# Optimization experiments

Measured on AMD Instinct MI355X. Metric: run time of the kernel, lower is better.

## Reference

```python
import jax, jax.numpy as jnp
import numpy as np

NUM_HEADS = 32
HEAD_DIM = 128
NUM_KV_HEADS = 8
SCALE = 1.0 / np.sqrt(HEAD_DIM)
BATCH = 8
SEQ = 1024
TOTAL = BATCH * SEQ


def setup_inputs() -> dict:
    key = jax.random.key(0)
    kq, kk, kv = jax.random.split(key, 3)
    q = jax.random.normal(kq, (TOTAL, NUM_HEADS * HEAD_DIM), dtype=jnp.float32)
    k = jax.random.normal(kk, (TOTAL, NUM_KV_HEADS * HEAD_DIM), dtype=jnp.float32)
    v = jax.random.normal(kv, (TOTAL, NUM_KV_HEADS * HEAD_DIM), dtype=jnp.float32)
    cu = (jnp.arange(BATCH + 1, dtype=jnp.int32) * SEQ)
    return {"q": q, "k": k, "v": v, "cu_seqlens_q": cu, "cu_seqlens_k": cu}


def reference(q, k, v, cu_seqlens_q, cu_seqlens_k):
    # Prefill path of Attention.forward: causal varlen GQA flash attention.
    # Equal-length sequences -> reshape flat tokens into [B, S, ...].
    B = cu_seqlens_q.shape[0] - 1          # static: number of sequences
    T = q.shape[0]
    S = T // B
    G = NUM_HEADS // NUM_KV_HEADS          # query heads per kv head
    qr = q.reshape(B, S, NUM_KV_HEADS, G, HEAD_DIM)
    kr = k.reshape(B, S, NUM_KV_HEADS, HEAD_DIM)
    vr = v.reshape(B, S, NUM_KV_HEADS, HEAD_DIM)
    # scores: [B, Hkv, G, Sq, Sk]
    scores = jnp.einsum('bqhgd,bkhd->bhgqk', qr, kr) * jnp.float32(SCALE)
    causal = jnp.tril(jnp.ones((S, S), dtype=bool))  # [Sq, Sk]
    scores = jnp.where(causal, scores, jnp.finfo(scores.dtype).min)
    probs = jax.nn.softmax(scores, axis=-1)
    o = jnp.einsum('bhgqk,bkhd->bqhgd', probs, vr)
    return o.reshape(T, NUM_HEADS * HEAD_DIM)
```

## Files before the change

kernel.cpp:

```cpp
#include <hip/hip_runtime.h>
#include <hip/hip_bf16.h>
#include <stdint.h>

typedef __bf16 bf16_t;
typedef __attribute__((ext_vector_type(8))) __bf16 bf16x8;
typedef __attribute__((ext_vector_type(4))) __bf16 bf16x4;
typedef __attribute__((ext_vector_type(4))) float f32x4;

#define NHEADS 32
#define HDIM 128
#define NKV 8
#define GQ 4
#define BATCH 8
#define SEQ 1024
#define TOTAL (BATCH * SEQ)
#define QD (NHEADS * HDIM)
#define KVD (NKV * HDIM)
#define ATT_SCALE 0.08838834764831845f
#define QSCL (0.08838834764831845f * 1.4426950408889634f)

#define QBLK 64
#define KBLK 64
#define NQT (SEQ / QBLK)

__device__ __forceinline__ void gload16(const bf16_t* g, bf16_t* l) {
    __builtin_amdgcn_global_load_lds(
        (const __attribute__((address_space(1))) void*)g,
        (__attribute__((address_space(3))) void*)l,
        16, 0, 0);
}

__device__ __forceinline__ uint32_t cvt_pk_bf16(float lo, float hi) {
    uint32_t r;
    asm("v_cvt_pk_bf16_f32 %0, %1, %2" : "=v"(r) : "v"(lo), "v"(hi));
    return r;
}

__global__ __launch_bounds__(256)
void attn_prepass_kernel(const float* __restrict__ kg, const float* __restrict__ vg,
                         bf16_t* __restrict__ kws, bf16_t* __restrict__ vtws)
{
    const int bid = blockIdx.x;
    const int tid = threadIdx.x;
    if (bid < 512) {
        __shared__ bf16_t Lt[128 * 130];
        const int b  = bid >> 6;
        const int hk = (bid >> 3) & 7;
        const int tt = bid & 7;
        const float* vp = vg + ((long)(b * SEQ + tt * 128)) * KVD + hk * HDIM;
        #pragma unroll
        for (int it = 0; it < 16; ++it) {
            int idx = it * 256 + tid;
            int t  = idx >> 5;
            int c4 = (idx & 31) * 4;
            float4 f = *(const float4*)(vp + (long)t * KVD + c4);
            Lt[(c4 + 0) * 130 + t] = (bf16_t)f.x;
            Lt[(c4 + 1) * 130 + t] = (bf16_t)f.y;
            Lt[(c4 + 2) * 130 + t] = (bf16_t)f.z;
            Lt[(c4 + 3) * 130 + t] = (bf16_t)f.w;
        }
        __syncthreads();
        bf16_t* op = vtws + ((long)((b * NKV + hk) * HDIM)) * SEQ + tt * 128;
        #pragma unroll
        for (int jt = 0; jt < 8; ++jt) {
            int jdx = jt * 256 + tid;
            int d  = jdx >> 4;
            int c8 = (jdx & 15) * 8;
            const bf16_t* lp = &Lt[d * 130 + c8];
            uint32_t u0 = *(const uint32_t*)(lp + 0);
            uint32_t u1 = *(const uint32_t*)(lp + 2);
            uint32_t u2 = *(const uint32_t*)(lp + 4);
            uint32_t u3 = *(const uint32_t*)(lp + 6);
            int kl0 = c8 & 63;
            int p0  = (kl0 & 32) | ((kl0 & 8) << 1) | ((kl0 & 16) >> 2);
            bf16_t* dst = op + (long)d * SEQ + (c8 & ~63);
            uint2 lo; lo.x = u0; lo.y = u1;
            uint2 hi; hi.x = u2; hi.y = u3;
            *(uint2*)(dst + p0)     = lo;
            *(uint2*)(dst + p0 + 8) = hi;
        }
    } else {
        const long total4 = (long)TOTAL * KVD / 4;
        const float4* k4 = (const float4*)kg;
        for (long i = (long)(bid - 512) * 256 + tid; i < total4; i += 1024L * 256) {
            float4 f = k4[i];
            bf16x4 o4;
            o4[0] = (bf16_t)f.x; o4[1] = (bf16_t)f.y;
            o4[2] = (bf16_t)f.z; o4[3] = (bf16_t)f.w;
            *(bf16x4*)(kws + i * 4) = o4;
        }
    }
}

__global__ __launch_bounds__(512, 4)
void attn_fwd_v11(const float* __restrict__ qg, const bf16_t* __restrict__ kws,
                  const bf16_t* __restrict__ vtws, float* __restrict__ og)
{
    __shared__ __align__(16) bf16_t Kl[2][KBLK * HDIM];
    __shared__ __align__(16) bf16_t Vl[2][HDIM * KBLK];

    const int tid  = threadIdx.x;
    const int w    = tid >> 6;
    const int lane = tid & 63;
    const int l16  = lane & 15;
    const int l4   = lane >> 4;

    const int bid = blockIdx.x;
    const int hg  = bid & 1;
    const int bh  = (bid >> 1) & 63;
    const int pi  = bid >> 7;
    const int b   = bh >> 3;
    const int hk  = bh & 7;
    const int g2  = w >> 2;
    const int fs  = w & 3;
    const int h   = hk * GQ + hg * 2 + g2;

    const bf16_t* kbase = kws + (long)(b * SEQ) * KVD + hk * HDIM;
    const bf16_t* vbase = vtws + (long)((b * NKV + hk) * HDIM) * SEQ;
    const int kc0 = w * 2;

    long koff[2], voff[2];
    int ldst[2];
    #pragma unroll
    for (int i = 0; i < 2; ++i) {
        int c = kc0 + i;
        int r = c * 4 + (lane >> 4);
        koff[i] = (long)r * KVD + (((lane & 15) ^ (r & 7)) * 8);
        int d = c * 8 + (lane >> 3);
        voff[i] = (long)d * SEQ + (((lane & 7) ^ (d & 7)) * 8);
        ldst[i] = c * 512;
    }
    const long KT_STRIDE = (long)KBLK * KVD;

    for (int ph = 0; ph < 2; ++ph) {
        const int qt = ph ? pi : (NQT - 1 - pi);
        const long qtok0 = (long)b * SEQ + qt * QBLK;

        bf16x8 aq[4];
        {
            const float* qp = qg + (qtok0 + fs * 16 + l16) * QD + h * HDIM + l4 * 8;
            #pragma unroll
            for (int s = 0; s < 4; ++s) {
                float4 x = *(const float4*)(qp + s * 32);
                float4 y = *(const float4*)(qp + s * 32 + 4);
                bf16x8 t;
                t[0] = (bf16_t)(x.x * QSCL); t[1] = (bf16_t)(x.y * QSCL);
                t[2] = (bf16_t)(x.z * QSCL); t[3] = (bf16_t)(x.w * QSCL);
                t[4] = (bf16_t)(y.x * QSCL); t[5] = (bf16_t)(y.y * QSCL);
                t[6] = (bf16_t)(y.z * QSCL); t[7] = (bf16_t)(y.w * QSCL);
                aq[s] = t;
            }
        }
        __builtin_amdgcn_sched_barrier(0);
        __syncthreads();

        f32x4 accO[8];
        #pragma unroll
        for (int n = 0; n < 8; ++n) accO[n] = (f32x4){0.f, 0.f, 0.f, 0.f};
        float rsum[4] = {0.f, 0.f, 0.f, 0.f};

        const bf16_t* kn = kbase;
        const bf16_t* vn = vbase;
        auto issue_tile = [&](int buf) {
            gload16(kn + koff[0], &Kl[buf][ldst[0]]);
            gload16(kn + koff[1], &Kl[buf][ldst[1]]);
            gload16(vn + voff[0], &Vl[buf][ldst[0]]);
            gload16(vn + voff[1], &Vl[buf][ldst[1]]);
            kn += KT_STRIDE;
            vn += KBLK;
        };

        const int nkt = qt + 1;
        issue_tile(0);

        for (int kt = 0; kt < nkt; ++kt) {
            const bf16_t* Kc = &Kl[kt & 1][0];
            const bf16_t* Vc = &Vl[kt & 1][0];
            asm volatile("s_waitcnt vmcnt(0)" ::: "memory");
            __builtin_amdgcn_s_barrier();
            if (kt + 1 < nkt) issue_tile((kt + 1) & 1);
            __builtin_amdgcn_sched_barrier(0);

            const bool diag = (kt == qt);

            uint32_t u[4][2];
            #pragma unroll
            for (int kb = 0; kb < 4; ++kb) { u[kb][0] = 0; u[kb][1] = 0; }

            #pragma unroll
            for (int kb = 0; kb < 4; ++kb) {
                const bool skip = diag && (kb > fs);
                if (!skip) {
                    f32x4 t = (f32x4){0.f, 0.f, 0.f, 0.f};
                    __builtin_amdgcn_s_setprio(1);
                    #pragma unroll
                    for (int s = 0; s < 4; ++s) {
                        int elem = (s * 32 + l4 * 8) ^ ((l16 & 7) << 3);
                        bf16x8 bk = *(const bf16x8*)(Kc + (kb * 16 + l16) * 128 + elem);
                        t = __builtin_amdgcn_mfma_f32_16x16x32_bf16(bk, aq[s], t, 0, 0, 0);
                    }
                    __builtin_amdgcn_s_setprio(0);
                    const bool needmask = diag && (kb == fs);
                    #pragma unroll
                    for (int j = 0; j < 4; ++j) {
                        float p = exp2f(t[j]);
                        if (needmask && (kb * 16 + l4 * 4 + j > fs * 16 + l16)) p = 0.f;
                        t[j] = p;
                        rsum[j] += p;
                    }
                    u[kb][0] = cvt_pk_bf16(t[0], t[1]);
                    u[kb][1] = cvt_pk_bf16(t[2], t[3]);
                }
            }

            bf16x8 pa[2];
            #pragma unroll
            for (int ks = 0; ks < 2; ++ks) {
                union { uint32_t uu[4]; bf16x8 v; } pk;
                pk.uu[0] = u[ks * 2][0];
                pk.uu[1] = u[ks * 2][1];
                pk.uu[2] = u[ks * 2 + 1][0];
                pk.uu[3] = u[ks * 2 + 1][1];
                pa[ks] = pk.v;
            }

            __builtin_amdgcn_s_setprio(1);
            #pragma unroll
            for (int n = 0; n < 8; ++n) {
                #pragma unroll
                for (int ks = 0; ks < 2; ++ks) {
                    int elem = (ks * 32 + l4 * 8) ^ ((l16 & 7) << 3);
                    bf16x8 bv = *(const bf16x8*)(Vc + (n * 16 + l16) * 64 + elem);
                    accO[n] = __builtin_amdgcn_mfma_f32_16x16x32_bf16(pa[ks], bv, accO[n], 0, 0, 0);
                }
            }
            __builtin_amdgcn_s_setprio(0);
        }

        float rs = (rsum[0] + rsum[1]) + (rsum[2] + rsum[3]);
        rs += __shfl_xor(rs, 16);
        rs += __shfl_xor(rs, 32);
        float inv = 1.f / rs;
        #pragma unroll
        for (int j = 0; j < 4; ++j) {
            const int qr = l4 * 4 + j;
            float invr = __shfl(inv, qr);
            float* op = og + (qtok0 + fs * 16 + qr) * QD + h * HDIM + l16;
            #pragma unroll
            for (int n = 0; n < 8; ++n)
                op[n * 16] = accO[n][j] * invr;
        }
    }
}

#define KPAD 136
#define VPAD 72
#define PPAD 72
__global__ __launch_bounds__(512, 2)
void attn_fwd_v1(const float* __restrict__ qg, const float* __restrict__ kg,
                 const float* __restrict__ vg, float* __restrict__ og)
{
    __shared__ bf16_t Kl[KBLK * KPAD];
    __shared__ bf16_t Vt[HDIM * VPAD];
    __shared__ bf16_t Pl[8 * 16 * PPAD];

    const int tid  = threadIdx.x;
    const int w    = tid >> 6;
    const int lane = tid & 63;
    const int l4   = lane >> 4;
    const int l16  = lane & 15;

    const int bid = blockIdx.x;
    const int bh  = bid % 64;
    const int qt  = (NQT - 1) - bid / 64;
    const int b   = bh / NKV;
    const int hk  = bh % NKV;
    const int g   = w >> 1;
    const int h   = hk * GQ + g;
    const int rh  = (w & 1) * 32;

    const long qtok0 = (long)b * SEQ + qt * QBLK;

    bf16x8 aq[2][4];
    #pragma unroll
    for (int f = 0; f < 2; ++f) {
        const float* qp = qg + (qtok0 + rh + f * 16 + l16) * QD + h * HDIM + l4 * 8;
        #pragma unroll
        for (int s = 0; s < 4; ++s) {
            float4 x = *(const float4*)(qp + s * 32);
            float4 y = *(const float4*)(qp + s * 32 + 4);
            bf16x8 t;
            t[0] = (bf16_t)x.x; t[1] = (bf16_t)x.y; t[2] = (bf16_t)x.z; t[3] = (bf16_t)x.w;
            t[4] = (bf16_t)y.x; t[5] = (bf16_t)y.y; t[6] = (bf16_t)y.z; t[7] = (bf16_t)y.w;
            aq[f][s] = t;
        }
    }

    f32x4 accO[2][8];
    float mrun[2][4], lsum[2][4];
    #pragma unroll
    for (int f = 0; f < 2; ++f) {
        #pragma unroll
        for (int n = 0; n < 8; ++n) accO[f][n] = (f32x4){0.f, 0.f, 0.f, 0.f};
        #pragma unroll
        for (int j = 0; j < 4; ++j) { mrun[f][j] = -1e30f; lsum[f][j] = 0.f; }
    }

    const long ktok0 = (long)b * SEQ;
    const int nkt = qt + 1;

    for (int kt = 0; kt < nkt; ++kt) {
        __syncthreads();
        const float* kp = kg + (ktok0 + kt * KBLK) * KVD + hk * HDIM;
        const float* vp = vg + (ktok0 + kt * KBLK) * KVD + hk * HDIM;
        #pragma unroll
        for (int it = 0; it < 4; ++it) {
            int idx = it * 512 + tid;
            int row = idx >> 5;
            int c4  = (idx & 31) * 4;
            float4 kf = *(const float4*)(kp + (long)row * KVD + c4);
            bf16x4 k4;
            k4[0] = (bf16_t)kf.x; k4[1] = (bf16_t)kf.y; k4[2] = (bf16_t)kf.z; k4[3] = (bf16_t)kf.w;
            *(bf16x4*)(&Kl[row * KPAD + c4]) = k4;
            float4 vf = *(const float4*)(vp + (long)row * KVD + c4);
            const float* vfa = (const float*)&vf;
            #pragma unroll
            for (int m = 0; m < 4; ++m) {
                int d   = c4 + m;
                int blk = (row >> 3) ^ ((d >> 3) & 7);
                Vt[d * VPAD + blk * 8 + (row & 7)] = (bf16_t)vfa[m];
            }
        }
        __syncthreads();

        const bool diag = (kt == qt);
        bf16_t* pw = &Pl[w * 16 * PPAD];

        #pragma unroll
        for (int f = 0; f < 2; ++f) {
            f32x4 accS[4];
            #pragma unroll
            for (int n = 0; n < 4; ++n) {
                f32x4 acc = (f32x4){0.f, 0.f, 0.f, 0.f};
                #pragma unroll
                for (int s = 0; s < 4; ++s) {
                    bf16x8 bk = *(const bf16x8*)(&Kl[(n * 16 + l16) * KPAD + s * 32 + l4 * 8]);
                    acc = __builtin_amdgcn_mfma_f32_16x16x32_bf16(aq[f][s], bk, acc, 0, 0, 0);
                }
                accS[n] = acc;
            }

            const int qrow_loc = rh + f * 16 + l4 * 4;
            float pm[4];
            #pragma unroll
            for (int j = 0; j < 4; ++j) pm[j] = -1e30f;
            #pragma unroll
            for (int n = 0; n < 4; ++n) {
                #pragma unroll
                for (int j = 0; j < 4; ++j) {
                    float sv = accS[n][j] * ATT_SCALE;
                    if (diag && (n * 16 + l16 > qrow_loc + j)) sv = -1e30f;
                    accS[n][j] = sv;
                    pm[j] = fmaxf(pm[j], sv);
                }
            }
            #pragma unroll
            for (int j = 0; j < 4; ++j) {
                float m0 = pm[j];
                m0 = fmaxf(m0, __shfl_xor(m0, 1));
                m0 = fmaxf(m0, __shfl_xor(m0, 2));
                m0 = fmaxf(m0, __shfl_xor(m0, 4));
                m0 = fmaxf(m0, __shfl_xor(m0, 8));
                pm[j] = m0;
            }
            float al[4], rs[4];
            #pragma unroll
            for (int j = 0; j < 4; ++j) {
                float mnew = fmaxf(mrun[f][j], pm[j]);
                al[j] = __expf(mrun[f][j] - mnew);
                mrun[f][j] = mnew;
                rs[j] = 0.f;
            }
            #pragma unroll
            for (int n = 0; n < 4; ++n) {
                #pragma unroll
                for (int j = 0; j < 4; ++j) {
                    float p = __expf(accS[n][j] - mrun[f][j]);
                    accS[n][j] = p;
                    rs[j] += p;
                }
            }
            #pragma unroll
            for (int j = 0; j < 4; ++j) {
                float r = rs[j];
                r += __shfl_xor(r, 1);
                r += __shfl_xor(r, 2);
                r += __shfl_xor(r, 4);
                r += __shfl_xor(r, 8);
                lsum[f][j] = lsum[f][j] * al[j] + r;
            }
            #pragma unroll
            for (int n = 0; n < 8; ++n) {
                #pragma unroll
                for (int j = 0; j < 4; ++j) accO[f][n][j] *= al[j];
            }
            #pragma unroll
            for (int n = 0; n < 4; ++n) {
                #pragma unroll
                for (int j = 0; j < 4; ++j)
                    pw[(l4 * 4 + j) * PPAD + n * 16 + l16] = (bf16_t)accS[n][j];
            }
            asm volatile("s_waitcnt lgkmcnt(0)" ::: "memory");
            __builtin_amdgcn_sched_barrier(0);
            #pragma unroll
            for (int ks = 0; ks < 2; ++ks) {
                bf16x8 ap = *(const bf16x8*)(&pw[l16 * PPAD + ks * 32 + l4 * 8]);
                #pragma unroll
                for (int n = 0; n < 8; ++n) {
                    int d   = n * 16 + l16;
                    int blk = (ks * 4 + l4) ^ ((d >> 3) & 7);
                    bf16x8 bv = *(const bf16x8*)(&Vt[d * VPAD + blk * 8]);
                    accO[f][n] = __builtin_amdgcn_mfma_f32_16x16x32_bf16(ap, bv, accO[f][n], 0, 0, 0);
                }
            }
        }
    }

    #pragma unroll
    for (int f = 0; f < 2; ++f) {
        #pragma unroll
        for (int j = 0; j < 4; ++j) {
            float inv = 1.f / lsum[f][j];
            float* op = og + (qtok0 + rh + f * 16 + l4 * 4 + j) * QD + h * HDIM;
            #pragma unroll
            for (int n = 0; n < 8; ++n)
                op[n * 16 + l16] = accO[f][n][j] * inv;
        }
    }
}

extern "C" void kernel_launch(void* const* d_in, const int* in_sizes, int n_in,
                              void* d_out, int out_size, void* d_ws, size_t ws_size,
                              hipStream_t stream) {
    const float* q = (const float*)d_in[0];
    const float* k = (const float*)d_in[1];
    const float* v = (const float*)d_in[2];
    float* o = (float*)d_out;

    const size_t kws_elems = (size_t)TOTAL * KVD;
    const size_t vws_elems = (size_t)BATCH * NKV * HDIM * SEQ;
    const size_t need = (kws_elems + vws_elems) * sizeof(bf16_t);

    if (ws_size >= need) {
        bf16_t* kws  = (bf16_t*)d_ws;
        bf16_t* vtws = kws + kws_elems;
        attn_prepass_kernel<<<1536, 256, 0, stream>>>(k, v, kws, vtws);
        attn_fwd_v11<<<1024, 512, 0, stream>>>(q, kws, vtws, o);
    } else {
        attn_fwd_v1<<<NQT * BATCH * NKV, 512, 0, stream>>>(q, k, v, o);
    }
}
```

Before: 145.9 us.

## Process two query heads per wave to reuse K/V LDS fragments

The attention block shrinks from 8 waves to 4, and each wave now handles two GQA query heads that share one KV head. Every K and V fragment read from LDS feeds two MFMAs instead of one, which halves LDS read traffic per FLOP. The cost is doubled accumulator and Q register state per wave (accO 2x8, aq 2x4), fewer waves per block, and a launch bound of 2, all of which can cut occupancy and latency hiding.

```diff
diff --git a/kernel.cpp b/kernel.cpp
--- a/kernel.cpp
+++ b/kernel.cpp
@@ -92,8 +92,8 @@
     }
 }
 
-__global__ __launch_bounds__(512, 4)
-void attn_fwd_v11(const float* __restrict__ qg, const bf16_t* __restrict__ kws,
+__global__ __launch_bounds__(256, 2)
+void attn_fwd_v12(const float* __restrict__ qg, const bf16_t* __restrict__ kws,
                   const bf16_t* __restrict__ vtws, float* __restrict__ og)
 {
     __shared__ __align__(16) bf16_t Kl[2][KBLK * HDIM];
@@ -106,24 +106,22 @@
     const int l4   = lane >> 4;
 
     const int bid = blockIdx.x;
-    const int hg  = bid & 1;
+    const int hp  = bid & 1;
     const int bh  = (bid >> 1) & 63;
     const int pi  = bid >> 7;
     const int b   = bh >> 3;
     const int hk  = bh & 7;
-    const int g2  = w >> 2;
-    const int fs  = w & 3;
-    const int h   = hk * GQ + hg * 2 + g2;
+    const int fs  = w;
+    const int h0  = hk * GQ + hp * 2;
 
     const bf16_t* kbase = kws + (long)(b * SEQ) * KVD + hk * HDIM;
     const bf16_t* vbase = vtws + (long)((b * NKV + hk) * HDIM) * SEQ;
-    const int kc0 = w * 2;
-
-    long koff[2], voff[2];
-    int ldst[2];
+
+    long koff[4], voff[4];
+    int ldst[4];
     #pragma unroll
-    for (int i = 0; i < 2; ++i) {
-        int c = kc0 + i;
+    for (int i = 0; i < 4; ++i) {
+        int c = w * 4 + i;
         int r = c * 4 + (lane >> 4);
         koff[i] = (long)r * KVD + (((lane & 15) ^ (r & 7)) * 8);
         int d = c * 8 + (lane >> 3);
@@ -136,9 +134,10 @@
         const int qt = ph ? pi : (NQT - 1 - pi);
         const long qtok0 = (long)b * SEQ + qt * QBLK;
 
-        bf16x8 aq[4];
-        {
-            const float* qp = qg + (qtok0 + fs * 16 + l16) * QD + h * HDIM + l4 * 8;
+        bf16x8 aq[2][4];
+        #pragma unroll
+        for (int hh = 0; hh < 2; ++hh) {
+            const float* qp = qg + (qtok0 + fs * 16 + l16) * QD + (h0 + hh) * HDIM + l4 * 8;
             #pragma unroll
             for (int s = 0; s < 4; ++s) {
                 float4 x = *(const float4*)(qp + s * 32);
@@ -148,24 +147,30 @@
                 t[2] = (bf16_t)(x.z * QSCL); t[3] = (bf16_t)(x.w * QSCL);
                 t[4] = (bf16_t)(y.x * QSCL); t[5] = (bf16_t)(y.y * QSCL);
                 t[6] = (bf16_t)(y.z * QSCL); t[7] = (bf16_t)(y.w * QSCL);
-                aq[s] = t;
+                aq[hh][s] = t;
             }
         }
         __builtin_amdgcn_sched_barrier(0);
         __syncthreads();
 
-        f32x4 accO[8];
-        #pragma unroll
-        for (int n = 0; n < 8; ++n) accO[n] = (f32x4){0.f, 0.f, 0.f, 0.f};
-        float rsum[4] = {0.f, 0.f, 0.f, 0.f};
+        f32x4 accO[2][8];
+        #pragma unroll
+        for (int hh = 0; hh < 2; ++hh)
+            #pragma unroll
+            for (int n = 0; n < 8; ++n) accO[hh][n] = (f32x4){0.f, 0.f, 0.f, 0.f};
+        float rsum[2][4];
+        #pragma unroll
+        for (int hh = 0; hh < 2; ++hh)
+            #pragma unroll
+            for (int j = 0; j < 4; ++j) rsum[hh][j] = 0.f;
 
         const bf16_t* kn = kbase;
         const bf16_t* vn = vbase;
         auto issue_tile = [&](int buf) {
-            gload16(kn + koff[0], &Kl[buf][ldst[0]]);
-            gload16(kn + koff[1], &Kl[buf][ldst[1]]);
-            gload16(vn + voff[0], &Vl[buf][ldst[0]]);
-            gload16(vn + voff[1], &Vl[buf][ldst[1]]);
+            #pragma unroll
+            for (int i = 0; i < 4; ++i) gload16(kn + koff[i], &Kl[buf][ldst[i]]);
+            #pragma unroll
+            for (int i = 0; i < 4; ++i) gload16(vn + voff[i], &Vl[buf][ldst[i]]);
             kn += KT_STRIDE;
             vn += KBLK;
         };
@@ -183,45 +188,57 @@
 
             const bool diag = (kt == qt);
 
-            uint32_t u[4][2];
-            #pragma unroll
-            for (int kb = 0; kb < 4; ++kb) { u[kb][0] = 0; u[kb][1] = 0; }
+            uint32_t u[2][4][2];
+            #pragma unroll
+            for (int hh = 0; hh < 2; ++hh)
+                #pragma unroll
+                for (int kb = 0; kb < 4; ++kb) { u[hh][kb][0] = 0; u[hh][kb][1] = 0; }
 
             #pragma unroll
             for (int kb = 0; kb < 4; ++kb) {
                 const bool skip = diag && (kb > fs);
                 if (!skip) {
-                    f32x4 t = (f32x4){0.f, 0.f, 0.f, 0.f};
+                    f32x4 t0 = (f32x4){0.f, 0.f, 0.f, 0.f};
+                    f32x4 t1 = (f32x4){0.f, 0.f, 0.f, 0.f};
                     __builtin_amdgcn_s_setprio(1);
                     #pragma unroll
                     for (int s = 0; s < 4; ++s) {
                         int elem = (s * 32 + l4 * 8) ^ ((l16 & 7) << 3);
                         bf16x8 bk = *(const bf16x8*)(Kc + (kb * 16 + l16) * 128 + elem);
-                        t = __builtin_amdgcn_mfma_f32_16x16x32_bf16(bk, aq[s], t, 0, 0, 0);
+                        t0 = __builtin_amdgcn_mfma_f32_16x16x32_bf16(bk, aq[0][s], t0, 0, 0, 0);
+                        t1 = __builtin_amdgcn_mfma_f32_16x16x32_bf16(bk, aq[1][s], t1, 0, 0, 0);
                     }
                     __builtin_amdgcn_s_setprio(0);
                     const bool needmask = diag && (kb == fs);
                     #pragma unroll
                     for (int j = 0; j < 4; ++j) {
-                        float p = exp2f(t[j]);
-                        if (needmask && (kb * 16 + l4 * 4 + j > fs * 16 + l16)) p = 0.f;
-                        t[j] = p;
-                        rsum[j] += p;
+                        const bool m = needmask && (kb * 16 + l4 * 4 + j > fs * 16 + l16);
+                        float p0 = exp2f(t0[j]);
+                        float p1 = exp2f(t1[j]);
+                        if (m) { p0 = 0.f; p1 = 0.f; }
+                        t0[j] = p0; t1[j] = p1;
+                        rsum[0][j] += p0;
+                        rsum[1][j] += p1;
                     }
-                    u[kb][0] = cvt_pk_bf16(t[0], t[1]);
-                    u[kb][1] = cvt_pk_bf16(t[2], t[3]);
-                }
-            }
-
-            bf16x8 pa[2];
-            #pragma unroll
-            for (int ks = 0; ks < 2; ++ks) {
-                union { uint32_t uu[4]; bf16x8 v; } pk;
-                pk.uu[0] = u[ks * 2][0];
-                pk.uu[1] = u[ks * 2][1];
-                pk.uu[2] = u[ks * 2 + 1][0];
-                pk.uu[3] = u[ks * 2 + 1][1];
-                pa[ks] = pk.v;
+                    u[0][kb][0] = cvt_pk_bf16(t0[0], t0[1]);
+                    u[0][kb][1] = cvt_pk_bf16(t0[2], t0[3]);
+                    u[1][kb][0] = cvt_pk_bf16(t1[0], t1[1]);
+                    u[1][kb][1] = cvt_pk_bf16(t1[2], t1[3]);
+                }
+            }
+
+            bf16x8 pa[2][2];
+            #pragma unroll
+            for (int hh = 0; hh < 2; ++hh) {
+                #pragma unroll
+                for (int ks = 0; ks < 2; ++ks) {
+                    union { uint32_t uu[4]; bf16x8 v; } pk;
+                    pk.uu[0] = u[hh][ks * 2][0];
+                    pk.uu[1] = u[hh][ks * 2][1];
+                    pk.uu[2] = u[hh][ks * 2 + 1][0];
+                    pk.uu[3] = u[hh][ks * 2 + 1][1];
+                    pa[hh][ks] = pk.v;
+                }
             }
 
             __builtin_amdgcn_s_setprio(1);
@@ -231,24 +248,28 @@
                 for (int ks = 0; ks < 2; ++ks) {
                     int elem = (ks * 32 + l4 * 8) ^ ((l16 & 7) << 3);
                     bf16x8 bv = *(const bf16x8*)(Vc + (n * 16 + l16) * 64 + elem);
-                    accO[n] = __builtin_amdgcn_mfma_f32_16x16x32_bf16(pa[ks], bv, accO[n], 0, 0, 0);
+                    accO[0][n] = __builtin_amdgcn_mfma_f32_16x16x32_bf16(pa[0][ks], bv, accO[0][n], 0, 0, 0);
+                    accO[1][n] = __builtin_amdgcn_mfma_f32_16x16x32_bf16(pa[1][ks], bv, accO[1][n], 0, 0, 0);
                 }
             }
             __builtin_amdgcn_s_setprio(0);
         }
 
-        float rs = (rsum[0] + rsum[1]) + (rsum[2] + rsum[3]);
-        rs += __shfl_xor(rs, 16);
-        rs += __shfl_xor(rs, 32);
-        float inv = 1.f / rs;
-        #pragma unroll
-        for (int j = 0; j < 4; ++j) {
-            const int qr = l4 * 4 + j;
-            float invr = __shfl(inv, qr);
-            float* op = og + (qtok0 + fs * 16 + qr) * QD + h * HDIM + l16;
-            #pragma unroll
-            for (int n = 0; n < 8; ++n)
-                op[n * 16] = accO[n][j] * invr;
+        #pragma unroll
+        for (int hh = 0; hh < 2; ++hh) {
+            float rs = (rsum[hh][0] + rsum[hh][1]) + (rsum[hh][2] + rsum[hh][3]);
+            rs += __shfl_xor(rs, 16);
+            rs += __shfl_xor(rs, 32);
+            float inv = 1.f / rs;
+            #pragma unroll
+            for (int j = 0; j < 4; ++j) {
+                const int qr = l4 * 4 + j;
+                float invr = __shfl(inv, qr);
+                float* op = og + (qtok0 + fs * 16 + qr) * QD + (h0 + hh) * HDIM + l16;
+                #pragma unroll
+                for (int n = 0; n < 8; ++n)
+                    op[n * 16] = accO[hh][n][j] * invr;
+            }
         }
     }
 }
@@ -455,7 +476,7 @@
         bf16_t* kws  = (bf16_t*)d_ws;
         bf16_t* vtws = kws + kws_elems;
         attn_prepass_kernel<<<1536, 256, 0, stream>>>(k, v, kws, vtws);
-        attn_fwd_v11<<<1024, 512, 0, stream>>>(q, kws, vtws, o);
+        attn_fwd_v12<<<1024, 256, 0, stream>>>(q, kws, vtws, o);
     } else {
         attn_fwd_v1<<<NQT * BATCH * NKV, 512, 0, stream>>>(q, k, v, o);
     }
```

Measured after the change: 147.0 us. About the same (+0.8%).

## Use 1024-thread blocks covering all four GQA heads with 128-key tiles

Applied to the files above, without the earlier changes.

Each workgroup now processes all four query heads that share a KV head (16 waves, 1024 threads) instead of two, so K/V tiles staged in LDS are reused by twice as many waves. The key tile grows from 64 to 128 rows, halving the number of barrier/load iterations, and the causal diagonal logic is adapted to the larger tile. In exchange, LDS per block doubles to 128KB, grid size halves to 512 blocks, occupancy falls to one block per CU, and the diagonal tile wastes more masked work on odd query tiles.

```diff
diff --git a/kernel.cpp b/kernel.cpp
--- a/kernel.cpp
+++ b/kernel.cpp
@@ -21,6 +21,7 @@
 
 #define QBLK 64
 #define KBLK 64
+#define KT2 128
 #define NQT (SEQ / QBLK)
 
 __device__ __forceinline__ void gload16(const bf16_t* g, bf16_t* l) {
@@ -92,12 +93,12 @@
     }
 }
 
-__global__ __launch_bounds__(512, 4)
-void attn_fwd_v11(const float* __restrict__ qg, const bf16_t* __restrict__ kws,
+__global__ __launch_bounds__(1024)
+void attn_fwd_v13(const float* __restrict__ qg, const bf16_t* __restrict__ kws,
                   const bf16_t* __restrict__ vtws, float* __restrict__ og)
 {
-    __shared__ __align__(16) bf16_t Kl[2][KBLK * HDIM];
-    __shared__ __align__(16) bf16_t Vl[2][HDIM * KBLK];
+    __shared__ __align__(16) bf16_t Kl[2][KT2 * HDIM];
+    __shared__ __align__(16) bf16_t Vl[2][HDIM * KT2];
 
     const int tid  = threadIdx.x;
     const int w    = tid >> 6;
@@ -106,31 +107,30 @@
     const int l4   = lane >> 4;
 
     const int bid = blockIdx.x;
-    const int hg  = bid & 1;
-    const int bh  = (bid >> 1) & 63;
-    const int pi  = bid >> 7;
+    const int bh  = bid & 63;
+    const int pi  = bid >> 6;
     const int b   = bh >> 3;
     const int hk  = bh & 7;
-    const int g2  = w >> 2;
+    const int g   = w >> 2;
     const int fs  = w & 3;
-    const int h   = hk * GQ + hg * 2 + g2;
+    const int h   = hk * GQ + g;
 
     const bf16_t* kbase = kws + (long)(b * SEQ) * KVD + hk * HDIM;
     const bf16_t* vbase = vtws + (long)((b * NKV + hk) * HDIM) * SEQ;
-    const int kc0 = w * 2;
 
     long koff[2], voff[2];
     int ldst[2];
     #pragma unroll
     for (int i = 0; i < 2; ++i) {
-        int c = kc0 + i;
+        int c = w * 2 + i;
         int r = c * 4 + (lane >> 4);
         koff[i] = (long)r * KVD + (((lane & 15) ^ (r & 7)) * 8);
-        int d = c * 8 + (lane >> 3);
-        voff[i] = (long)d * SEQ + (((lane & 7) ^ (d & 7)) * 8);
+        int d  = c * 4 + (lane >> 4);
+        int e0 = (lane & 15) * 8;
+        voff[i] = (long)d * SEQ + (e0 & 64) + ((e0 & 63) ^ ((d & 7) << 3));
         ldst[i] = c * 512;
     }
-    const long KT_STRIDE = (long)KBLK * KVD;
+    const long KT_STRIDE = (long)KT2 * KVD;
 
     for (int ph = 0; ph < 2; ++ph) {
         const int qt = ph ? pi : (NQT - 1 - pi);
@@ -167,10 +167,11 @@
             gload16(vn + voff[0], &Vl[buf][ldst[0]]);
             gload16(vn + voff[1], &Vl[buf][ldst[1]]);
             kn += KT_STRIDE;
-            vn += KBLK;
+            vn += KT2;
         };
 
-        const int nkt = qt + 1;
+        const int nkt  = (qt >> 1) + 1;
+        const int dqfs = ((qt & 1) << 2) + fs;
         issue_tile(0);
 
         for (int kt = 0; kt < nkt; ++kt) {
@@ -181,15 +182,15 @@
             if (kt + 1 < nkt) issue_tile((kt + 1) & 1);
             __builtin_amdgcn_sched_barrier(0);
 
-            const bool diag = (kt == qt);
-
-            uint32_t u[4][2];
-            #pragma unroll
-            for (int kb = 0; kb < 4; ++kb) { u[kb][0] = 0; u[kb][1] = 0; }
-
-            #pragma unroll
-            for (int kb = 0; kb < 4; ++kb) {
-                const bool skip = diag && (kb > fs);
+            const bool diag = (kt == nkt - 1);
+
+            uint32_t u[8][2];
+            #pragma unroll
+            for (int kb = 0; kb < 8; ++kb) { u[kb][0] = 0; u[kb][1] = 0; }
+
+            #pragma unroll
+            for (int kb = 0; kb < 8; ++kb) {
+                const bool skip = diag && (kb > dqfs);
                 if (!skip) {
                     f32x4 t = (f32x4){0.f, 0.f, 0.f, 0.f};
                     __builtin_amdgcn_s_setprio(1);
@@ -200,11 +201,11 @@
                         t = __builtin_amdgcn_mfma_f32_16x16x32_bf16(bk, aq[s], t, 0, 0, 0);
                     }
                     __builtin_amdgcn_s_setprio(0);
-                    const bool needmask = diag && (kb == fs);
+                    const bool needmask = diag && (kb == dqfs);
                     #pragma unroll
                     for (int j = 0; j < 4; ++j) {
                         float p = exp2f(t[j]);
-                        if (needmask && (kb * 16 + l4 * 4 + j > fs * 16 + l16)) p = 0.f;
+                        if (needmask && (l4 * 4 + j > l16)) p = 0.f;
                         t[j] = p;
                         rsum[j] += p;
                     }
@@ -213,9 +214,9 @@
                 }
             }
 
-            bf16x8 pa[2];
-            #pragma unroll
-            for (int ks = 0; ks < 2; ++ks) {
+            bf16x8 pa[4];
+            #pragma unroll
+            for (int ks = 0; ks < 4; ++ks) {
                 union { uint32_t uu[4]; bf16x8 v; } pk;
                 pk.uu[0] = u[ks * 2][0];
                 pk.uu[1] = u[ks * 2][1];
@@ -228,9 +229,9 @@
             #pragma unroll
             for (int n = 0; n < 8; ++n) {
                 #pragma unroll
-                for (int ks = 0; ks < 2; ++ks) {
-                    int elem = (ks * 32 + l4 * 8) ^ ((l16 & 7) << 3);
-                    bf16x8 bv = *(const bf16x8*)(Vc + (n * 16 + l16) * 64 + elem);
+                for (int ks = 0; ks < 4; ++ks) {
+                    int elem = (((ks & 1) * 32 + l4 * 8) ^ ((l16 & 7) << 3)) + ((ks >> 1) * 64);
+                    bf16x8 bv = *(const bf16x8*)(Vc + (n * 16 + l16) * 128 + elem);
                     accO[n] = __builtin_amdgcn_mfma_f32_16x16x32_bf16(pa[ks], bv, accO[n], 0, 0, 0);
                 }
             }
@@ -455,7 +456,7 @@
         bf16_t* kws  = (bf16_t*)d_ws;
         bf16_t* vtws = kws + kws_elems;
         attn_prepass_kernel<<<1536, 256, 0, stream>>>(k, v, kws, vtws);
-        attn_fwd_v11<<<1024, 512, 0, stream>>>(q, kws, vtws, o);
+        attn_fwd_v13<<<512, 1024, 0, stream>>>(q, kws, vtws, o);
     } else {
         attn_fwd_v1<<<NQT * BATCH * NKV, 512, 0, stream>>>(q, k, v, o);
     }
```

Result: slower. 174.5 us (+19.6%).
